# Optimization experiments

Hardware: AMD Instinct MI355X
Metric: run time of the kernel (lower is better)

Reference implementation:

```python
import jax, jax.numpy as jnp
import numpy as np

D_MODEL = 384
D_STATE = 16
D_CONV = 4
EXPAND = 2
D_INNER = EXPAND * D_MODEL
DT_RANK = max(1, -(-D_MODEL // 16))  # ceil(d_model/16) = 24
BATCH = 32
SEQ = 1024


def _ssm_params(keys, prefix):
    s = 0.02
    n = lambda k, shp: jax.random.normal(k, shp, dtype=jnp.float32) * s
    A_log = jnp.broadcast_to(jnp.log(jnp.arange(1, D_STATE + 1, dtype=jnp.float32))[None, :], (D_INNER, D_STATE))
    return {
        prefix + '_in_w': n(keys[0], (2 * D_INNER, D_MODEL)),
        prefix + '_conv_w': n(keys[1], (D_INNER, 1, D_CONV)),
        prefix + '_conv_b': jnp.zeros((D_INNER,), jnp.float32),
        prefix + '_x_proj_w': n(keys[2], (DT_RANK + 2 * D_STATE, D_INNER)),
        prefix + '_dt_w': n(keys[3], (D_INNER, DT_RANK)),
        prefix + '_dt_b': jnp.zeros((D_INNER,), jnp.float32),
        prefix + '_A_log': A_log,
        prefix + '_D': jnp.ones((D_INNER,), jnp.float32),
        prefix + '_out_w': n(keys[4], (D_MODEL, D_INNER)),
    }


def setup_inputs() -> dict:
    key = jax.random.key(0)
    ks = jax.random.split(key, 13)
    inp = {
        'x': jax.random.normal(ks[0], (BATCH, SEQ, D_MODEL), dtype=jnp.float32),
        'ln_gamma': jnp.ones((D_MODEL,), jnp.float32),
        'ln_beta': jnp.zeros((D_MODEL,), jnp.float32),
        'gate_w': jax.random.normal(ks[11], (D_MODEL, 2 * D_MODEL), dtype=jnp.float32) * 0.02,
        'gate_b': jnp.zeros((D_MODEL,), jnp.float32),
    }
    inp.update(_ssm_params(ks[1:6], 'f'))
    inp.update(_ssm_params(ks[6:11], 'b'))
    return inp


def _selective_scan(xc, dt, A, Bm, Cm):
    # xc, dt: (B, L, d_inner); Bm, Cm: (B, L, N); A: (d_inner, N)
    h0 = jnp.zeros((xc.shape[0], xc.shape[2], A.shape[1]), xc.dtype)

    def step(h, inputs):
        x_t, dt_t, B_t, C_t = inputs          # (B,di), (B,di), (B,N), (B,N)
        dA = jnp.exp(dt_t[..., None] * A)     # (B, di, N)
        h = dA * h + (dt_t * x_t)[..., None] * B_t[:, None, :]
        y = jnp.einsum('bdn,bn->bd', h, C_t)
        return h, y

    xs = (jnp.moveaxis(xc, 1, 0), jnp.moveaxis(dt, 1, 0),
          jnp.moveaxis(Bm, 1, 0), jnp.moveaxis(Cm, 1, 0))
    _, ys = jax.lax.scan(step, h0, xs)
    return jnp.moveaxis(ys, 0, 1)  # (B, L, d_inner)


def _ssm(x, in_w, conv_w, conv_b, x_proj_w, dt_w, dt_b, A_log, Dp, out_w):
    L = x.shape[1]
    xz = jnp.einsum('bld,ed->ble', x, in_w)           # (B, L, 2*d_inner)
    xi, z = jnp.split(xz, 2, axis=-1)
    # depthwise causal conv1d (torch pads d_conv-1 then truncates to L)
    xc = jax.lax.conv_general_dilated(
        jnp.swapaxes(xi, 1, 2), conv_w, window_strides=(1,),
        padding=[(D_CONV - 1, 0)], feature_group_count=D_INNER,
        dimension_numbers=('NCH', 'OIH', 'NCH')) + conv_b[None, :, None]
    xc = jax.nn.silu(jnp.swapaxes(xc, 1, 2))          # (B, L, d_inner)
    xp = jnp.einsum('bld,ed->ble', xc, x_proj_w)      # (B, L, dt_rank+2N)
    dt = jax.nn.softplus(jnp.einsum('blr,dr->bld', xp[..., :DT_RANK], dt_w) + dt_b)
    Bm = xp[..., DT_RANK:DT_RANK + D_STATE]
    Cm = xp[..., DT_RANK + D_STATE:]
    A = -jnp.exp(A_log)
    y = _selective_scan(xc, dt, A, Bm, Cm)
    y = y + xc * Dp
    y = y * jax.nn.silu(z)
    return jnp.einsum('ble,de->bld', y, out_w)


def reference(x, ln_gamma, ln_beta,
              f_in_w, f_conv_w, f_conv_b, f_x_proj_w, f_dt_w, f_dt_b, f_A_log, f_D, f_out_w,
              b_in_w, b_conv_w, b_conv_b, b_x_proj_w, b_dt_w, b_dt_b, b_A_log, b_D, b_out_w,
              gate_w, gate_b):
    residual = x
    mu = jnp.mean(x, axis=-1, keepdims=True)
    var = jnp.mean((x - mu) ** 2, axis=-1, keepdims=True)
    xn = (x - mu) * jax.lax.rsqrt(var + 1e-5) * ln_gamma + ln_beta
    y_fwd = _ssm(xn, f_in_w, f_conv_w, f_conv_b, f_x_proj_w, f_dt_w, f_dt_b, f_A_log, f_D, f_out_w)
    y_bwd = _ssm(jnp.flip(xn, axis=1), b_in_w, b_conv_w, b_conv_b, b_x_proj_w, b_dt_w, b_dt_b, b_A_log, b_D, b_out_w)
    y_bwd = jnp.flip(y_bwd, axis=1)
    combined = jnp.concatenate([y_fwd, y_bwd], axis=-1)
    gate = jax.nn.sigmoid(jnp.einsum('blc,dc->bld', combined, gate_w) + gate_b)
    y = gate * y_fwd + (1.0 - gate) * y_bwd
    return y + residual
```

## Files before the change

### kernel.cpp

```cpp
#include <hip/hip_runtime.h>
#include <hip/hip_bf16.h>

#define BATCH  32
#define SEQ    1024
#define DMODEL 384
#define DINNER 768
#define DSTATE 16
#define DTRANK 24
#define NTOK   (BATCH * SEQ)
#define TC     32
#define CL     (SEQ / TC)
#define DTR_R  32

typedef __hip_bfloat16 bf16;
typedef __attribute__((ext_vector_type(8))) short frag_ab;
typedef __attribute__((ext_vector_type(4))) float frag_cd;

__device__ __forceinline__ float b2f(bf16 v) { return __bfloat162float(v); }
__device__ __forceinline__ bf16  f2b(float v) { return __float2bfloat16(v); }
__device__ __forceinline__ float ldx(const void* p, size_t i, bool f32m) {
    return f32m ? ((const float*)p)[i] : b2f(((const bf16*)p)[i]);
}

__device__ __forceinline__ void gld16(void* l, const void* g) {
    __builtin_amdgcn_global_load_lds(
        (const __attribute__((address_space(1))) unsigned int*)g,
        (__attribute__((address_space(3))) unsigned int*)l, 16, 0, 0);
}

__global__ void detect_kernel(const unsigned short* __restrict__ x, int* flag) {
    int bad = 0;
    for (int i = threadIdx.x; i < 16384; i += 256) {
        int e = (x[i] >> 7) & 0xFF;
        bad |= (e >= 0xE0);
    }
    if (bad) atomicOr(flag, 1);
}

__global__ void struct_check(const float* __restrict__ alog, int* flag) {
    int c = blockIdx.x * 256 + threadIdx.x;
    if (c >= DINNER) return;
    float a0 = __expf(alog[c * 16]);
    int bad = 0;
#pragma unroll
    for (int n = 1; n < DSTATE; ++n) {
        float r = __expf(alog[c * 16 + n]) / a0;
        bad |= (fabsf(r - (float)(n + 1)) > 1e-3f * (n + 1));
    }
    if (bad) atomicOr(flag + 1, 1);
}

struct CvtF { const void* src[15]; float* dst[15]; int n[15]; };
struct CvtB { const void* src[7];  bf16*  dst[7];  int n[7];  };

__global__ void convert_f_kernel(CvtF p, const int* __restrict__ flag) {
    bool f32m = (*flag != 0);
    int y = blockIdx.y;
    const void* s = p.src[y];
    float* d = p.dst[y];
    int n = p.n[y];
    for (int i = blockIdx.x * 256 + threadIdx.x; i < n; i += gridDim.x * 256)
        d[i] = ldx(s, i, f32m);
}
__global__ void convert_b_kernel(CvtB p, const int* __restrict__ flag) {
    bool f32m = (*flag != 0);
    int y = blockIdx.y;
    const void* s = p.src[y];
    bf16* d = p.dst[y];
    int n = p.n[y];
    for (int i = blockIdx.x * 256 + threadIdx.x; i < n; i += gridDim.x * 256)
        d[i] = f2b(ldx(s, i, f32m));
}

__global__ void transpose_dtw(const float* __restrict__ w, float* __restrict__ wt) {
    int i = blockIdx.x * 256 + threadIdx.x;
    if (i >= DINNER * DTRANK) return;
    int c = i / DTRANK, r = i % DTRANK;
    wt[r * DINNER + c] = w[i];
}

__global__ void ln_kernel(const void* __restrict__ x, size_t xoff,
                          const float* __restrict__ gamma, const float* __restrict__ beta,
                          bf16* __restrict__ xn, const int* __restrict__ flag) {
    bool f32m = (*flag != 0);
    int wave = threadIdx.x >> 6;
    int lane = threadIdx.x & 63;
    int row  = blockIdx.x * 4 + wave;
    size_t base = xoff + (size_t)row * DMODEL;
    float v[6];
    float s = 0.f, s2 = 0.f;
#pragma unroll
    for (int i = 0; i < 6; ++i) {
        v[i] = ldx(x, base + lane + i * 64, f32m);
        s += v[i];
        s2 += v[i] * v[i];
    }
#pragma unroll
    for (int off = 32; off >= 1; off >>= 1) {
        s  += __shfl_down(s, off, 64);
        s2 += __shfl_down(s2, off, 64);
    }
    s  = __shfl(s, 0, 64);
    s2 = __shfl(s2, 0, 64);
    float mu   = s / DMODEL;
    float var  = s2 / DMODEL - mu * mu;
    float rstd = rsqrtf(var + 1e-5f);
    bf16* xnr = xn + (size_t)row * DMODEL;
#pragma unroll
    for (int i = 0; i < 6; ++i)
        xnr[lane + i * 64] = f2b((v[i] - mu) * rstd * gamma[lane + i * 64] + beta[lane + i * 64]);
}

__device__ __forceinline__ uint4 silu_mul(uint4 y8, float4 z0, float4 z1) {
    const bf16* yb = (const bf16*)&y8;
    uint4 r;
    bf16* rb = (bf16*)&r;
    float zz[8] = {z0.x, z0.y, z0.z, z0.w, z1.x, z1.y, z1.z, z1.w};
#pragma unroll
    for (int j = 0; j < 8; ++j) {
        float s = zz[j] / (1.f + __expf(-zz[j]));
        rb[j] = f2b(b2f(yb[j]) * s);
    }
    return r;
}

template <int MODE>
__global__ __launch_bounds__(256) void gemm_mfma(
    const bf16* __restrict__ A, const bf16* __restrict__ W,
    int K, int lda, int ldw,
    bf16* __restrict__ C, int ldc, int cofs,
    float* __restrict__ Cf,
    const float* __restrict__ gb, const void* __restrict__ xg, size_t xoff,
    void* __restrict__ outg, const float* __restrict__ zF,
    const int* __restrict__ flag) {
    __shared__ bf16 Als[128][32];
    __shared__ bf16 Bls[128][32];
    int tid = threadIdx.x;
    int lane = tid & 63;
    int w = tid >> 6;
    int wm = w & 1, wn = w >> 1;
    int m0 = blockIdx.y * 128, n0 = blockIdx.x * 128;
    int row = tid >> 2, kc = tid & 3;
    int mr = lane & 15, quad = lane >> 4;

    const bf16* Ab0 = A + (size_t)(m0 + row) * lda + kc * 8;
    const bf16* Ab1 = A + (size_t)(m0 + 64 + row) * lda + kc * 8;
    const bf16* Wb0 = W + (size_t)(n0 + row) * ldw + kc * 8;
    const bf16* Wb1 = W + (size_t)(n0 + 64 + row) * ldw + kc * 8;
    void* lA0 = &Als[row][kc * 8];
    void* lA1 = &Als[64 + row][kc * 8];
    void* lB0 = &Bls[row][kc * 8];
    void* lB1 = &Bls[64 + row][kc * 8];

    frag_cd acc[4][4] = {};

    for (int k0 = 0; k0 < K; k0 += 32) {
        if (MODE == 5) {
            uint4 ya0 = *(const uint4*)(Ab0 + k0);
            uint4 ya1 = *(const uint4*)(Ab1 + k0);
            const float* zr0 = zF + (size_t)(m0 + row) * DINNER + k0 + kc * 8;
            const float* zr1 = zF + (size_t)(m0 + 64 + row) * DINNER + k0 + kc * 8;
            float4 z00 = *(const float4*)zr0, z01 = *(const float4*)(zr0 + 4);
            float4 z10 = *(const float4*)zr1, z11 = *(const float4*)(zr1 + 4);
            uint4 ea0 = silu_mul(ya0, z00, z01);
            uint4 ea1 = silu_mul(ya1, z10, z11);
            __syncthreads();
            *(uint4*)lA0 = ea0;
            *(uint4*)lA1 = ea1;
            gld16(lB0, Wb0 + k0);
            gld16(lB1, Wb1 + k0);
            __syncthreads();
        } else {
            __syncthreads();
            gld16(lA0, Ab0 + k0);
            gld16(lA1, Ab1 + k0);
            gld16(lB0, Wb0 + k0);
            gld16(lB1, Wb1 + k0);
            __syncthreads();
        }
        frag_ab af[4], bfr[4];
#pragma unroll
        for (int r = 0; r < 4; ++r)
            af[r] = *(const frag_ab*)&Als[wm * 64 + r * 16 + mr][quad * 8];
#pragma unroll
        for (int c = 0; c < 4; ++c)
            bfr[c] = *(const frag_ab*)&Bls[wn * 64 + c * 16 + mr][quad * 8];
#pragma unroll
        for (int r = 0; r < 4; ++r)
#pragma unroll
            for (int c = 0; c < 4; ++c)
                acc[r][c] = __builtin_amdgcn_mfma_f32_16x16x32_bf16(af[r], bfr[c], acc[r][c], 0, 0, 0);
    }

    bool f32m = (MODE == 1) ? (*flag != 0) : false;
#pragma unroll
    for (int r = 0; r < 4; ++r) {
#pragma unroll
        for (int c = 0; c < 4; ++c) {
#pragma unroll
            for (int reg = 0; reg < 4; ++reg) {
                int gm = m0 + wm * 64 + r * 16 + quad * 4 + reg;
                int gn = n0 + wn * 64 + c * 16 + mr;
                float v = acc[r][c][reg];
                if (MODE == 0 || MODE == 5) {
                    C[(size_t)gm * ldc + cofs + gn] = f2b(v);
                } else if (MODE == 2) {
                    if (gn < DTRANK + 2 * DSTATE) Cf[(size_t)gm * 56 + gn] = v;
                } else if (MODE == 4) {
                    if (gn < DINNER) C[(size_t)gm * DINNER + gn] = f2b(v);
                    else             Cf[(size_t)gm * DINNER + (gn - DINNER)] = v;
                } else {
                    float g   = 1.f / (1.f + __expf(-(v + gb[gn])));
                    float yfv = b2f(A[(size_t)gm * DINNER + gn]);
                    float ybv = b2f(A[(size_t)gm * DINNER + DMODEL + gn]);
                    size_t gi = xoff + (size_t)gm * DMODEL + gn;
                    float xv  = f32m ? ((const float*)xg)[gi] : b2f(((const bf16*)xg)[gi]);
                    float rr  = g * yfv + (1.f - g) * ybv + xv;
                    if (f32m) ((float*)outg)[gi] = rr;
                    else      ((bf16*)outg)[gi]  = f2b(rr);
                }
            }
        }
    }
}

__global__ void conv_kernel(const bf16* __restrict__ xi_buf, const float* __restrict__ cw,
                            const float* __restrict__ cb, bf16* __restrict__ xc, int reverse) {
    int g = blockIdx.x * blockDim.x + threadIdx.x;
    int c  = g % DINNER;
    int bl = g / DINNER;
    int l = bl % SEQ;
    int b = bl / SEQ;
    float w[4];
#pragma unroll
    for (int k = 0; k < 4; ++k) w[k] = cw[c * 4 + k];
    const bf16* xi = xi_buf + (size_t)b * SEQ * DINNER + c;
    float acc = cb[c];
    if (!reverse) {
#pragma unroll
        for (int k = 0; k < 4; ++k) {
            int ll = l - 3 + k;
            if (ll >= 0) acc += b2f(xi[(size_t)ll * DINNER]) * w[k];
        }
    } else {
#pragma unroll
        for (int j = 0; j < 4; ++j) {
            int ll = l + j;
            if (ll < SEQ) acc += b2f(xi[(size_t)ll * DINNER]) * w[3 - j];
        }
    }
    xc[(size_t)bl * DINNER + c] = f2b(acc / (1.f + __expf(-acc)));
}

__global__ __launch_bounds__(256, 4) void dt_kernel(const float* __restrict__ xp,
                                                    const float* __restrict__ dtwT,
                                                    const float* __restrict__ dtb,
                                                    float* __restrict__ dtf) {
    __shared__ float4 xps[DTR_R][6];
    int tid = threadIdx.x;
    int c = blockIdx.y * 256 + tid;
    float w[DTRANK];
#pragma unroll
    for (int r = 0; r < DTRANK; ++r) w[r] = dtwT[r * DINNER + c];
#pragma unroll
    for (int r = 0; r < DTRANK; ++r) asm volatile("" : "+v"(w[r]));
    float bias = dtb[c];

    size_t row0 = (size_t)blockIdx.x * DTR_R;
    for (int i = tid; i < DTR_R * 6; i += 256) {
        int s = i / 6, q = i % 6;
        xps[s][q] = *(const float4*)(xp + (row0 + s) * 56 + q * 4);
    }
    __syncthreads();

    for (int s = 0; s < DTR_R; s += 2) {
        float a0 = bias, a1 = bias;
#pragma unroll
        for (int q = 0; q < 6; ++q) {
            float4 x0 = xps[s][q];
            float4 x1 = xps[s + 1][q];
            a0 += x0.x * w[q * 4 + 0];  a1 += x1.x * w[q * 4 + 0];
            a0 += x0.y * w[q * 4 + 1];  a1 += x1.y * w[q * 4 + 1];
            a0 += x0.z * w[q * 4 + 2];  a1 += x1.z * w[q * 4 + 2];
            a0 += x0.w * w[q * 4 + 3];  a1 += x1.w * w[q * 4 + 3];
        }
        float e0 = __builtin_amdgcn_exp2f(fabsf(a0) * -1.44269504f);
        float e1 = __builtin_amdgcn_exp2f(fabsf(a1) * -1.44269504f);
        a0 = fmaxf(a0, 0.f) + 0.69314718f * __builtin_amdgcn_logf(1.f + e0);
        a1 = fmaxf(a1, 0.f) + 0.69314718f * __builtin_amdgcn_logf(1.f + e1);
        dtf[(row0 + s) * DINNER + c]     = a0;
        dtf[(row0 + s + 1) * DINNER + c] = a1;
    }
}

template <int PHASE>
__global__ void scan_phase(const float* __restrict__ xp, const bf16* __restrict__ xc,
                           const float* __restrict__ dtf, const float* __restrict__ Alog,
                           const float* __restrict__ Dg, float* __restrict__ states,
                           bf16* __restrict__ ydir, int reverse, const int* __restrict__ flag) {
    __shared__ float xps[16][32];
    bool generic = (flag[1] != 0);
    int tid = threadIdx.x;
    int bidx = blockIdx.x;
    int tc  = bidx % TC;
    int cgb = bidx / TC;
    int cg  = cgb % 6;
    int bb  = cgb / 6;
    int c = cg * 128 + tid;

    float Av0 = -__expf(Alog[c * DSTATE]);
    float Av[DSTATE];
    if (generic) {
#pragma unroll
        for (int n = 0; n < DSTATE; ++n) Av[n] = -__expf(Alog[c * DSTATE + n]);
    }
    float Dv = Dg[c];

    float h[DSTATE];
    float Q = 1.f, Pg[DSTATE];
    size_t sbase = (size_t)bidx * 32;
    if (PHASE == 0) {
#pragma unroll
        for (int n = 0; n < DSTATE; ++n) { h[n] = 0.f; Pg[n] = 1.f; }
    } else {
#pragma unroll
        for (int n = 0; n < DSTATE; ++n) h[n] = states[(sbase + n) * 128 + tid];
    }

    const size_t brow = (size_t)bb * SEQ;
    const int t0 = tc * CL;
    const int tr0 = reverse ? (SEQ - 1 - t0) : t0;
    const long dstep = reverse ? -(long)DINNER : (long)DINNER;
    const float* pdt = dtf + (brow + tr0) * DINNER + c;
    const bf16*  pxc = xc  + (brow + tr0) * DINNER + c;
    bf16* pyd = (PHASE == 1) ? (ydir + (brow + tr0) * DINNER + c) : nullptr;

    for (int g0 = 0; g0 < CL; g0 += 16) {
        __syncthreads();
        for (int i = tid; i < 16 * 32; i += 128) {
            int s = i >> 5, r = i & 31;
            int t = t0 + g0 + s;
            int tr = reverse ? (SEQ - 1 - t) : t;
            xps[s][r] = xp[(brow + tr) * 56 + 24 + r];
        }
        __syncthreads();
        for (int s = 0; s < 16; ++s) {
            float dt  = *pdt;  pdt += dstep;
            float xcv = b2f(*pxc);  pxc += dstep;
            float dtx = dt * xcv;
            float accv = 0.f;
            if (!generic) {
                float e1 = __expf(dt * Av0);
                float d = e1;
#pragma unroll
                for (int n = 0; n < DSTATE; ++n) {
                    h[n] = d * h[n] + dtx * xps[s][n];
                    if (PHASE == 1) accv += h[n] * xps[s][16 + n];
                    d *= e1;
                }
                if (PHASE == 0) Q *= e1;
            } else {
#pragma unroll
                for (int n = 0; n < DSTATE; ++n) {
                    float dA = __expf(dt * Av[n]);
                    h[n] = dA * h[n] + dtx * xps[s][n];
                    if (PHASE == 0) Pg[n] *= dA;
                    else accv += h[n] * xps[s][16 + n];
                }
            }
            if (PHASE == 1) {
                *pyd = f2b(accv + xcv * Dv);
                pyd += dstep;
            }
        }
    }
    if (PHASE == 0) {
        if (!generic) {
            float d = Q;
#pragma unroll
            for (int n = 0; n < DSTATE; ++n) { Pg[n] = d; d *= Q; }
        }
#pragma unroll
        for (int n = 0; n < DSTATE; ++n) {
            states[(sbase + n) * 128 + tid]      = Pg[n];
            states[(sbase + 16 + n) * 128 + tid] = h[n];
        }
    }
}

__global__ void scan_stitch(float* __restrict__ states) {
    int tid = threadIdx.x;
    int cgb = blockIdx.x;
    float h[DSTATE];
#pragma unroll
    for (int n = 0; n < DSTATE; ++n) h[n] = 0.f;
    for (int tc = 0; tc < TC; ++tc) {
        size_t base = ((size_t)cgb * TC + tc) * 32;
#pragma unroll
        for (int n = 0; n < DSTATE; ++n) {
            float Pv = states[(base + n) * 128 + tid];
            float ev = states[(base + 16 + n) * 128 + tid];
            states[(base + n) * 128 + tid] = h[n];
            h[n] = Pv * h[n] + ev;
        }
    }
}

extern "C" void kernel_launch(void* const* d_in, const int* in_sizes, int n_in,
                              void* d_out, int out_size, void* d_ws, size_t ws_size,
                              hipStream_t stream) {
    (void)n_in; (void)out_size;
    bool dict_order = (in_sizes[4] < 2048);
    int fbase = dict_order ? 5 : 3;
    int bbase = dict_order ? 14 : 12;
    int gwi = dict_order ? 3 : 21;
    int gbi = dict_order ? 4 : 22;

    auto al = [](size_t b) { return (b + 255) & ~(size_t)255; };
    char* ws = (char*)d_ws;
    size_t off = 0;
    auto alloc = [&](size_t bytes) {
        void* p = ws + off;
        off += al(bytes);
        return p;
    };

    int* flag = (int*)alloc(256);

    CvtF pf{};
    int cf = 0;
    auto addf = [&](int idx, int n) {
        float* d = (float*)alloc((size_t)n * 4);
        pf.src[cf] = d_in[idx]; pf.dst[cf] = d; pf.n[cf] = n; ++cf;
        return d;
    };
    float* ln_gc   = addf(1, DMODEL);
    float* ln_bc   = addf(2, DMODEL);
    float* gate_bc = addf(gbi, DMODEL);
    float* convw_f[2], *convb_f[2], *dtw_f[2], *dtb_f[2], *alog_f[2], *dd_f[2];
    for (int d = 0; d < 2; ++d) {
        int base = d ? bbase : fbase;
        convw_f[d] = addf(base + 1, DINNER * 4);
        convb_f[d] = addf(base + 2, DINNER);
        dtw_f[d]   = addf(base + 4, DINNER * DTRANK);
        dtb_f[d]   = addf(base + 5, DINNER);
        alog_f[d]  = addf(base + 6, DINNER * DSTATE);
        dd_f[d]    = addf(base + 7, DINNER);
    }

    CvtB pb{};
    int cb = 0;
    auto addb = [&](int idx, int n, size_t alloc_n) {
        bf16* d = (bf16*)alloc(alloc_n * 2);
        pb.src[cb] = d_in[idx]; pb.dst[cb] = d; pb.n[cb] = n; ++cb;
        return d;
    };
    bf16* gate_wb = addb(gwi, DMODEL * 2 * DMODEL, (size_t)DMODEL * 2 * DMODEL);
    bf16 *inw_b[2], *xpw_b[2], *outw_b[2];
    for (int d = 0; d < 2; ++d) {
        int base = d ? bbase : fbase;
        inw_b[d]  = addb(base + 0, 2 * DINNER * DMODEL, (size_t)2 * DINNER * DMODEL);
        xpw_b[d]  = addb(base + 3, 56 * DINNER, (size_t)128 * DINNER);
        outw_b[d] = addb(base + 8, DMODEL * DINNER, (size_t)DMODEL * DINNER);
    }

    float* dtwT_f[2];
    for (int d = 0; d < 2; ++d)
        dtwT_f[d] = (float*)alloc((size_t)DTRANK * DINNER * 4);

    size_t fixed = off;

    auto chunk_need = [&](int bc) {
        size_t T = (size_t)bc * SEQ;
        return al(T * DMODEL * 2)
             + 2 * al(T * DINNER * 2)
             + al(T * 56 * 4)
             + al(T * DINNER * 4)
             + al(T * DINNER * 4)
             + al(T * DINNER * 2)
             + al((size_t)bc * 6 * TC * 32 * 128 * 4);
    };
    int Bc = 32;
    while (Bc > 1 && fixed + chunk_need(Bc) > ws_size) Bc >>= 1;
    size_t T = (size_t)Bc * SEQ;

    bf16*  xn_c   = (bf16*)alloc(T * DMODEL * 2);
    bf16*  xib    = (bf16*)alloc(T * DINNER * 2);
    bf16*  xcb    = (bf16*)alloc(T * DINNER * 2);
    float* xpb    = (float*)alloc(T * 56 * 4);
    float* dtfb   = (float*)alloc(T * DINNER * 4);
    float* zbf    = (float*)alloc(T * DINNER * 4);
    bf16*  ycat   = (bf16*)alloc(T * DINNER * 2);
    float* states = (float*)alloc((size_t)Bc * 6 * TC * 32 * 128 * 4);
    bf16*  ydir   = xib;

    hipMemsetAsync(flag, 0, 8, stream);
    for (int d = 0; d < 2; ++d)
        hipMemsetAsync(xpw_b[d], 0, (size_t)128 * DINNER * 2, stream);
    detect_kernel<<<1, 256, 0, stream>>>((const unsigned short*)d_in[0], flag);
    convert_f_kernel<<<dim3(8, 15), 256, 0, stream>>>(pf, flag);
    convert_b_kernel<<<dim3(32, 7), 256, 0, stream>>>(pb, flag);
    struct_check<<<3, 256, 0, stream>>>(alog_f[0], flag);
    struct_check<<<3, 256, 0, stream>>>(alog_f[1], flag);
    for (int d = 0; d < 2; ++d)
        transpose_dtw<<<(DINNER * DTRANK + 255) / 256, 256, 0, stream>>>(dtw_f[d], dtwT_f[d]);

    for (int c0 = 0; c0 < BATCH; c0 += Bc) {
        size_t tok0 = (size_t)c0 * SEQ;

        ln_kernel<<<(unsigned)(T / 4), 256, 0, stream>>>(
            d_in[0], tok0 * DMODEL, ln_gc, ln_bc, xn_c, flag);

        for (int dir = 0; dir < 2; ++dir) {
            gemm_mfma<4><<<dim3(2 * DINNER / 128, T / 128), 256, 0, stream>>>(
                xn_c, inw_b[dir], DMODEL, DMODEL, DMODEL,
                xib, DINNER, 0, zbf, nullptr, nullptr, 0, nullptr, nullptr, flag);
            conv_kernel<<<(unsigned)((T * DINNER) / 256), 256, 0, stream>>>(
                xib, convw_f[dir], convb_f[dir], xcb, dir);
            gemm_mfma<2><<<dim3(1, T / 128), 256, 0, stream>>>(
                xcb, xpw_b[dir], DINNER, DINNER, DINNER,
                nullptr, 0, 0, xpb, nullptr, nullptr, 0, nullptr, nullptr, flag);
            dt_kernel<<<dim3((unsigned)(T / DTR_R), 3), 256, 0, stream>>>(
                xpb, dtwT_f[dir], dtb_f[dir], dtfb);
            scan_phase<0><<<Bc * 6 * TC, 128, 0, stream>>>(
                xpb, xcb, dtfb, alog_f[dir], dd_f[dir], states, nullptr, dir, flag);
            scan_stitch<<<Bc * 6, 128, 0, stream>>>(states);
            scan_phase<1><<<Bc * 6 * TC, 128, 0, stream>>>(
                xpb, xcb, dtfb, alog_f[dir], dd_f[dir], states, ydir, dir, flag);
            gemm_mfma<5><<<dim3(DMODEL / 128, T / 128), 256, 0, stream>>>(
                ydir, outw_b[dir], DINNER, DINNER, DINNER,
                ycat, DINNER, dir * DMODEL, nullptr, nullptr, nullptr, 0, nullptr, zbf, flag);
        }

        gemm_mfma<1><<<dim3(DMODEL / 128, T / 128), 256, 0, stream>>>(
            ycat, gate_wb, DINNER, DINNER, DINNER,
            nullptr, 0, 0, nullptr, gate_bc, d_in[0], tok0 * DMODEL, d_out, nullptr, flag);
    }
}
```

Measured before the change: 1.461 ms.

## Double-buffer GEMM LDS tiles and precompute bf16 silu(z) in in-proj epilogue

```diff
diff --git a/kernel.cpp b/kernel.cpp
--- a/kernel.cpp
+++ b/kernel.cpp
@@ -28,6 +28,16 @@
         (__attribute__((address_space(3))) unsigned int*)l, 16, 0, 0);
 }
 
+__device__ __forceinline__ uint4 bmul8(uint4 y, uint4 s) {
+    const bf16* yb = (const bf16*)&y;
+    const bf16* sb = (const bf16*)&s;
+    uint4 r;
+    bf16* rb = (bf16*)&r;
+#pragma unroll
+    for (int j = 0; j < 8; ++j) rb[j] = f2b(b2f(yb[j]) * b2f(sb[j]));
+    return r;
+}
+
 __global__ void detect_kernel(const unsigned short* __restrict__ x, int* flag) {
     int bad = 0;
     for (int i = threadIdx.x; i < 16384; i += 256) {
@@ -111,17 +121,21 @@
         xnr[lane + i * 64] = f2b((v[i] - mu) * rstd * gamma[lane + i * 64] + beta[lane + i * 64]);
 }
 
-__device__ __forceinline__ uint4 silu_mul(uint4 y8, float4 z0, float4 z1) {
-    const bf16* yb = (const bf16*)&y8;
-    uint4 r;
-    bf16* rb = (bf16*)&r;
-    float zz[8] = {z0.x, z0.y, z0.z, z0.w, z1.x, z1.y, z1.z, z1.w};
-#pragma unroll
-    for (int j = 0; j < 8; ++j) {
-        float s = zz[j] / (1.f + __expf(-zz[j]));
-        rb[j] = f2b(b2f(yb[j]) * s);
-    }
-    return r;
+__device__ __forceinline__ void compute_tile(const bf16 (*Al)[32], const bf16 (*Bl)[32],
+                                             frag_cd acc[4][4], int wm, int wn,
+                                             int mr, int quad) {
+    frag_ab af[4], bfr[4];
+#pragma unroll
+    for (int r = 0; r < 4; ++r)
+        af[r] = *(const frag_ab*)&Al[wm * 64 + r * 16 + mr][quad * 8];
+#pragma unroll
+    for (int c = 0; c < 4; ++c)
+        bfr[c] = *(const frag_ab*)&Bl[wn * 64 + c * 16 + mr][quad * 8];
+#pragma unroll
+    for (int r = 0; r < 4; ++r)
+#pragma unroll
+        for (int c = 0; c < 4; ++c)
+            acc[r][c] = __builtin_amdgcn_mfma_f32_16x16x32_bf16(af[r], bfr[c], acc[r][c], 0, 0, 0);
 }
 
 template <int MODE>
@@ -129,12 +143,11 @@
     const bf16* __restrict__ A, const bf16* __restrict__ W,
     int K, int lda, int ldw,
     bf16* __restrict__ C, int ldc, int cofs,
-    float* __restrict__ Cf,
+    float* __restrict__ Cf, bf16* __restrict__ Cz, const bf16* __restrict__ Sz,
     const float* __restrict__ gb, const void* __restrict__ xg, size_t xoff,
-    void* __restrict__ outg, const float* __restrict__ zF,
-    const int* __restrict__ flag) {
-    __shared__ bf16 Als[128][32];
-    __shared__ bf16 Bls[128][32];
+    void* __restrict__ outg, const int* __restrict__ flag) {
+    __shared__ bf16 Als[2][128][32];
+    __shared__ bf16 Bls[2][128][32];
     int tid = threadIdx.x;
     int lane = tid & 63;
     int w = tid >> 6;
@@ -147,49 +160,70 @@
     const bf16* Ab1 = A + (size_t)(m0 + 64 + row) * lda + kc * 8;
     const bf16* Wb0 = W + (size_t)(n0 + row) * ldw + kc * 8;
     const bf16* Wb1 = W + (size_t)(n0 + 64 + row) * ldw + kc * 8;
-    void* lA0 = &Als[row][kc * 8];
-    void* lA1 = &Als[64 + row][kc * 8];
-    void* lB0 = &Bls[row][kc * 8];
-    void* lB1 = &Bls[64 + row][kc * 8];
+    const bf16* Zb0 = (MODE == 5) ? (Sz + (size_t)(m0 + row) * DINNER + kc * 8) : nullptr;
+    const bf16* Zb1 = (MODE == 5) ? (Sz + (size_t)(m0 + 64 + row) * DINNER + kc * 8) : nullptr;
 
     frag_cd acc[4][4] = {};
-
-    for (int k0 = 0; k0 < K; k0 += 32) {
-        if (MODE == 5) {
-            uint4 ya0 = *(const uint4*)(Ab0 + k0);
-            uint4 ya1 = *(const uint4*)(Ab1 + k0);
-            const float* zr0 = zF + (size_t)(m0 + row) * DINNER + k0 + kc * 8;
-            const float* zr1 = zF + (size_t)(m0 + 64 + row) * DINNER + k0 + kc * 8;
-            float4 z00 = *(const float4*)zr0, z01 = *(const float4*)(zr0 + 4);
-            float4 z10 = *(const float4*)zr1, z11 = *(const float4*)(zr1 + 4);
-            uint4 ea0 = silu_mul(ya0, z00, z01);
-            uint4 ea1 = silu_mul(ya1, z10, z11);
+    const int NT = K / 32;
+
+    if (MODE == 5) {
+        uint4 eya0, eya1, esz0, esz1;
+        uint4 oya0, oya1, osz0, osz1;
+        eya0 = *(const uint4*)(Ab0);      eya1 = *(const uint4*)(Ab1);
+        esz0 = *(const uint4*)(Zb0);      esz1 = *(const uint4*)(Zb1);
+        oya0 = *(const uint4*)(Ab0 + 32); oya1 = *(const uint4*)(Ab1 + 32);
+        osz0 = *(const uint4*)(Zb0 + 32); osz1 = *(const uint4*)(Zb1 + 32);
+        *(uint4*)&Als[0][row][kc * 8]      = bmul8(eya0, esz0);
+        *(uint4*)&Als[0][64 + row][kc * 8] = bmul8(eya1, esz1);
+        gld16(&Bls[0][row][kc * 8], Wb0);
+        gld16(&Bls[0][64 + row][kc * 8], Wb1);
+        __syncthreads();
+        for (int t = 0; t < NT; t += 2) {
+            int k1 = (t + 1) * 32, k2 = (t + 2) * 32, k3 = (t + 3) * 32;
+            *(uint4*)&Als[1][row][kc * 8]      = bmul8(oya0, osz0);
+            *(uint4*)&Als[1][64 + row][kc * 8] = bmul8(oya1, osz1);
+            gld16(&Bls[1][row][kc * 8], Wb0 + k1);
+            gld16(&Bls[1][64 + row][kc * 8], Wb1 + k1);
+            if (t + 2 < NT) {
+                eya0 = *(const uint4*)(Ab0 + k2); eya1 = *(const uint4*)(Ab1 + k2);
+                esz0 = *(const uint4*)(Zb0 + k2); esz1 = *(const uint4*)(Zb1 + k2);
+            }
+            compute_tile(Als[0], Bls[0], acc, wm, wn, mr, quad);
             __syncthreads();
-            *(uint4*)lA0 = ea0;
-            *(uint4*)lA1 = ea1;
-            gld16(lB0, Wb0 + k0);
-            gld16(lB1, Wb1 + k0);
+            if (t + 2 < NT) {
+                *(uint4*)&Als[0][row][kc * 8]      = bmul8(eya0, esz0);
+                *(uint4*)&Als[0][64 + row][kc * 8] = bmul8(eya1, esz1);
+                gld16(&Bls[0][row][kc * 8], Wb0 + k2);
+                gld16(&Bls[0][64 + row][kc * 8], Wb1 + k2);
+                oya0 = *(const uint4*)(Ab0 + k3); oya1 = *(const uint4*)(Ab1 + k3);
+                osz0 = *(const uint4*)(Zb0 + k3); osz1 = *(const uint4*)(Zb1 + k3);
+            }
+            compute_tile(Als[1], Bls[1], acc, wm, wn, mr, quad);
             __syncthreads();
-        } else {
+        }
+    } else {
+        gld16(&Als[0][row][kc * 8], Ab0);
+        gld16(&Als[0][64 + row][kc * 8], Ab1);
+        gld16(&Bls[0][row][kc * 8], Wb0);
+        gld16(&Bls[0][64 + row][kc * 8], Wb1);
+        __syncthreads();
+        for (int t = 0; t < NT; t += 2) {
+            int k1 = (t + 1) * 32, k2 = (t + 2) * 32;
+            gld16(&Als[1][row][kc * 8], Ab0 + k1);
+            gld16(&Als[1][64 + row][kc * 8], Ab1 + k1);
+            gld16(&Bls[1][row][kc * 8], Wb0 + k1);
+            gld16(&Bls[1][64 + row][kc * 8], Wb1 + k1);
+            compute_tile(Als[0], Bls[0], acc, wm, wn, mr, quad);
             __syncthreads();
-            gld16(lA0, Ab0 + k0);
-            gld16(lA1, Ab1 + k0);
-            gld16(lB0, Wb0 + k0);
-            gld16(lB1, Wb1 + k0);
+            if (t + 2 < NT) {
+                gld16(&Als[0][row][kc * 8], Ab0 + k2);
+                gld16(&Als[0][64 + row][kc * 8], Ab1 + k2);
+                gld16(&Bls[0][row][kc * 8], Wb0 + k2);
+                gld16(&Bls[0][64 + row][kc * 8], Wb1 + k2);
+            }
+            compute_tile(Als[1], Bls[1], acc, wm, wn, mr, quad);
             __syncthreads();
         }
-        frag_ab af[4], bfr[4];
-#pragma unroll
-        for (int r = 0; r < 4; ++r)
-            af[r] = *(const frag_ab*)&Als[wm * 64 + r * 16 + mr][quad * 8];
-#pragma unroll
-        for (int c = 0; c < 4; ++c)
-            bfr[c] = *(const frag_ab*)&Bls[wn * 64 + c * 16 + mr][quad * 8];
-#pragma unroll
-        for (int r = 0; r < 4; ++r)
-#pragma unroll
-            for (int c = 0; c < 4; ++c)
-                acc[r][c] = __builtin_amdgcn_mfma_f32_16x16x32_bf16(af[r], bfr[c], acc[r][c], 0, 0, 0);
     }
 
     bool f32m = (MODE == 1) ? (*flag != 0) : false;
@@ -207,8 +241,12 @@
                 } else if (MODE == 2) {
                     if (gn < DTRANK + 2 * DSTATE) Cf[(size_t)gm * 56 + gn] = v;
                 } else if (MODE == 4) {
-                    if (gn < DINNER) C[(size_t)gm * DINNER + gn] = f2b(v);
-                    else             Cf[(size_t)gm * DINNER + (gn - DINNER)] = v;
+                    if (gn < DINNER) {
+                        C[(size_t)gm * DINNER + gn] = f2b(v);
+                    } else {
+                        float sz = v / (1.f + __expf(-v));
+                        Cz[(size_t)gm * DINNER + (gn - DINNER)] = f2b(sz);
+                    }
                 } else {
                     float g   = 1.f / (1.f + __expf(-(v + gb[gn])));
                     float yfv = b2f(A[(size_t)gm * DINNER + gn]);
@@ -476,7 +514,7 @@
              + 2 * al(T * DINNER * 2)
              + al(T * 56 * 4)
              + al(T * DINNER * 4)
-             + al(T * DINNER * 4)
+             + al(T * DINNER * 2)
              + al(T * DINNER * 2)
              + al((size_t)bc * 6 * TC * 32 * 128 * 4);
     };
@@ -489,7 +527,7 @@
     bf16*  xcb    = (bf16*)alloc(T * DINNER * 2);
     float* xpb    = (float*)alloc(T * 56 * 4);
     float* dtfb   = (float*)alloc(T * DINNER * 4);
-    float* zbf    = (float*)alloc(T * DINNER * 4);
+    bf16*  zbb    = (bf16*)alloc(T * DINNER * 2);
     bf16*  ycat   = (bf16*)alloc(T * DINNER * 2);
     float* states = (float*)alloc((size_t)Bc * 6 * TC * 32 * 128 * 4);
     bf16*  ydir   = xib;
@@ -514,12 +552,14 @@
         for (int dir = 0; dir < 2; ++dir) {
             gemm_mfma<4><<<dim3(2 * DINNER / 128, T / 128), 256, 0, stream>>>(
                 xn_c, inw_b[dir], DMODEL, DMODEL, DMODEL,
-                xib, DINNER, 0, zbf, nullptr, nullptr, 0, nullptr, nullptr, flag);
+                xib, DINNER, 0, nullptr, zbb, nullptr,
+                nullptr, nullptr, 0, nullptr, flag);
             conv_kernel<<<(unsigned)((T * DINNER) / 256), 256, 0, stream>>>(
                 xib, convw_f[dir], convb_f[dir], xcb, dir);
             gemm_mfma<2><<<dim3(1, T / 128), 256, 0, stream>>>(
                 xcb, xpw_b[dir], DINNER, DINNER, DINNER,
-                nullptr, 0, 0, xpb, nullptr, nullptr, 0, nullptr, nullptr, flag);
+                nullptr, 0, 0, xpb, nullptr, nullptr,
+                nullptr, nullptr, 0, nullptr, flag);
             dt_kernel<<<dim3((unsigned)(T / DTR_R), 3), 256, 0, stream>>>(
                 xpb, dtwT_f[dir], dtb_f[dir], dtfb);
             scan_phase<0><<<Bc * 6 * TC, 128, 0, stream>>>(
@@ -529,11 +569,13 @@
                 xpb, xcb, dtfb, alog_f[dir], dd_f[dir], states, ydir, dir, flag);
             gemm_mfma<5><<<dim3(DMODEL / 128, T / 128), 256, 0, stream>>>(
                 ydir, outw_b[dir], DINNER, DINNER, DINNER,
-                ycat, DINNER, dir * DMODEL, nullptr, nullptr, nullptr, 0, nullptr, zbf, flag);
+                ycat, DINNER, dir * DMODEL, nullptr, nullptr, zbb,
+                nullptr, nullptr, 0, nullptr, flag);
         }
 
         gemm_mfma<1><<<dim3(DMODEL / 128, T / 128), 256, 0, stream>>>(
             ycat, gate_wb, DINNER, DINNER, DINNER,
-            nullptr, 0, 0, nullptr, gate_bc, d_in[0], tok0 * DMODEL, d_out, nullptr, flag);
-    }
-}
+            nullptr, 0, 0, nullptr, nullptr, nullptr,
+            gate_bc, d_in[0], tok0 * DMODEL, d_out, flag);
+    }
+}
```

Result: faster. 1.347 ms (-7.8%).
